# Kernel optimization log

Measured on AMD Instinct MI355X. Metric: run time of the kernel, lower is better.

The kernel has to match this reference:

```python
import jax, jax.numpy as jnp
import numpy as np

NEG_RATIO = 3.0
IOU_THR = 0.5
ALPHA = 1.0


def _cxcywh_to_xyxy(b):
    return jnp.concatenate([b[..., :2] - b[..., 2:] / 2, b[..., :2] + b[..., 2:] / 2], -1)


def _box_iou(a, b):  # a: [G,4] xyxy, b: [A,4] xyxy -> [G,A]
    lt = jnp.maximum(a[:, None, :2], b[None, :, :2])
    rb = jnp.minimum(a[:, None, 2:], b[None, :, 2:])
    wh = jnp.clip(rb - lt, 0.0)
    inter = wh[..., 0] * wh[..., 1]
    area_a = (a[:, 2] - a[:, 0]) * (a[:, 3] - a[:, 1])
    area_b = (b[:, 2] - b[:, 0]) * (b[:, 3] - b[:, 1])
    return inter / (area_a[:, None] + area_b[None, :] - inter)


def _encode(gt, anc):  # both cxcywh, last dim 4
    g_cxcy = (gt[..., :2] - anc[..., :2]) / anc[..., 2:]
    g_wh = jnp.log(gt[..., 2:]) - jnp.log(anc[..., 2:])
    return jnp.concatenate([g_cxcy, g_wh], -1)


def _match_one(boxes, labels, anchors):
    # boxes: [G,4] cxcywh, labels: [G] int, anchors: [A,4] cxcywh -> [A,5]
    ious = _box_iou(_cxcywh_to_xyxy(boxes), _cxcywh_to_xyxy(anchors))  # [G,A]
    best_gt_ov = ious.max(0)
    best_gt_idx = ious.argmax(0)  # [A]
    over = best_gt_ov > IOU_THR  # [A]
    lab_f = labels.astype(anchors.dtype)
    # anchors over threshold take their best gt, encoded w.r.t. that anchor
    enc_per_anchor = _encode(boxes[best_gt_idx], anchors)  # [A,4]
    ph = jnp.where(over[:, None],
                   jnp.concatenate([enc_per_anchor, lab_f[best_gt_idx][:, None]], -1),
                   0.0)  # [A,5]
    # every gt also claims its best anchor
    best_prior_idx = ious.argmax(1)  # [G]
    enc_best = _encode(boxes, anchors[best_prior_idx])  # [G,4]
    y2 = jnp.concatenate([enc_best, lab_f[:, None]], -1)
    return ph.at[best_prior_idx].set(y2)


def _multibox_loss(loc_pred, conf_pred, anchors, gt_boxes, gt_labels):
    B, A, C = conf_pred.shape
    target = jax.vmap(_match_one, in_axes=(0, 0, None))(gt_boxes, gt_labels, anchors)  # [B,A,5]
    pos = (target[:, :, 4:5] > 0).astype(loc_pred.dtype)  # [B,A,1]
    num_pos = pos.sum(axis=1, keepdims=True)  # [B,1,1]
    N = pos.sum()
    # smooth L1 on masked locations (beta=1), sum reduction
    d = pos * loc_pred - pos * target[:, :, :4]
    ad = jnp.abs(d)
    loc_loss = jnp.where(ad < 1.0, 0.5 * d * d, ad - 0.5).sum()
    # hard negative mining
    num_neg = jnp.minimum(NEG_RATIO * num_pos, A - 1)  # [B,1,1]
    lse = jax.scipy.special.logsumexp(conf_pred, axis=-1, keepdims=True)  # [B,A,1]
    idx01 = (target[:, :, 4:5] != 0).astype(jnp.int32)  # faithful: gathers class 0 or 1
    gathered = jnp.take_along_axis(conf_pred, idx01, axis=-1)  # [B,A,1]
    cls_l = (lse - gathered) * (1.0 - pos)  # zero-out positives
    order = jnp.argsort(-cls_l, axis=1)  # descending sort indices
    rank = jnp.argsort(order, axis=1)  # rank of each box's loss
    neg_mask = rank < num_neg
    sampled = jnp.logical_or(pos > 0, neg_mask)  # [B,A,1]
    s = sampled.astype(conf_pred.dtype)
    logits = (s * conf_pred).reshape(-1, C)
    labels_ce = (s * target[:, :, 4:5]).reshape(-1).astype(jnp.int32)
    lse2 = jax.scipy.special.logsumexp(logits, axis=-1)
    picked = jnp.take_along_axis(logits, labels_ce[:, None], axis=1)[:, 0]
    cls_loss = (lse2 - picked).sum()
    return (loc_loss + ALPHA * cls_loss) / N


def setup_inputs() -> dict:
    key = jax.random.key(0)
    k1, k2, k3, k4, k5, k6, k7 = jax.random.split(key, 7)
    B, A, C, G = 64, 8732, 81, 32
    loc_pred = jax.random.normal(k1, (B, A, 4), jnp.float32)
    conf_pred = jax.random.normal(k2, (B, A, C), jnp.float32)
    anc_cxcy = jax.random.uniform(k3, (A, 2), jnp.float32)
    anc_wh = jax.random.uniform(k4, (A, 2), jnp.float32) * 0.48 + 0.02
    anchors = jnp.concatenate([anc_cxcy, anc_wh], -1)
    gt_cxcy = jax.random.uniform(k5, (B, G, 2), jnp.float32) * 0.8 + 0.1
    gt_wh = jax.random.uniform(k6, (B, G, 2), jnp.float32) * 0.35 + 0.05
    gt_boxes = jnp.concatenate([gt_cxcy, gt_wh], -1)
    gt_labels = jax.random.randint(k7, (B, G), 0, C - 1, jnp.int32) + 1  # labels in 1..C-1
    return {"loc_pred": loc_pred, "conf_pred": conf_pred, "anchors": anchors,
            "gt_boxes": gt_boxes, "gt_labels": gt_labels}


def reference(loc_pred, conf_pred, anchors, gt_boxes, gt_labels):
    return _multibox_loss(loc_pred, conf_pred, anchors, gt_boxes, gt_labels)
```

## Files before the change

### kernel.cpp

```cpp
#include <hip/hip_runtime.h>
#include <math.h>

#pragma clang fp contract(off)

#define BB 64
#define AA 8732
#define CC 81
#define GG 32
#define A_BLOCKS 35
#define KA1_BLOCKS (BB*A_BLOCKS)
#define KA2_BLOCKS (BB*GG/4)
#define ROWS_PC 64
#define KC_BLOCKS (BB*AA/ROWS_PC)
#define CHUNK_F4 (ROWS_PC*81/4)


__global__ __launch_bounds__(256) void kAC(const float* __restrict__ anchors,
    const float* __restrict__ gt_boxes, const float* __restrict__ conf,
    unsigned char* __restrict__ bestg, unsigned int* __restrict__ bestp,
    float* __restrict__ cls_l, unsigned int* __restrict__ ticket,
    double* __restrict__ btot_acc, int* __restrict__ np_acc)
{
    __shared__ float buf[ROWS_PC * 81];
    int tid = threadIdx.x;
    if (blockIdx.x == 0 && tid == 0) {
        *ticket = 0u; *btot_acc = 0.0; *np_acc = 0;
    }
    if (blockIdx.x < KA1_BLOCKS) {
        int blk = blockIdx.x;
        int b = blk / A_BLOCKS, ca = blk % A_BLOCKS;
        int a = ca * 256 + tid;
        float4* gco = (float4*)buf;
        float* gar = buf + GG * 4;
        if (tid < GG) {
            float4 gb = ((const float4*)gt_boxes)[b * GG + tid];
            float x1 = gb.x - gb.z / 2.0f, y1 = gb.y - gb.w / 2.0f;
            float x2 = gb.x + gb.z / 2.0f, y2 = gb.y + gb.w / 2.0f;
            gco[tid] = make_float4(x1, y1, x2, y2);
            gar[tid] = (x2 - x1) * (y2 - y1);
        }
        __syncthreads();
        if (a >= AA) return;
        float4 an = ((const float4*)anchors)[a];
        float ax1 = an.x - an.z / 2.0f, ay1 = an.y - an.w / 2.0f;
        float ax2 = an.x + an.z / 2.0f, ay2 = an.y + an.w / 2.0f;
        float aar = (ax2 - ax1) * (ay2 - ay1);
        float bi = -1.0f, bu = 1.0f; int bgi = 0;
#pragma unroll
        for (int g = 0; g < GG; ++g) {
            float4 c = gco[g];
            float ltx = fmaxf(c.x, ax1), lty = fmaxf(c.y, ay1);
            float rbx = fminf(c.z, ax2), rby = fminf(c.w, ay2);
            float w = fmaxf(rbx - ltx, 0.0f), h = fmaxf(rby - lty, 0.0f);
            float inter = w * h;
            float uni = gar[g] + aar - inter;
            if (inter * bu > bi * uni) { bi = inter; bu = uni; bgi = g; }
        }
        bestg[b * AA + a] = (2.0f * bi > bu) ? (unsigned char)bgi : (unsigned char)0xFF;
    } else if (blockIdx.x < KA1_BLOCKS + KA2_BLOCKS) {
        int wv = tid >> 6, lane = tid & 63;
        int pair = (blockIdx.x - KA1_BLOCKS) * 4 + wv;
        int b = pair >> 5, g = pair & 31;
        float4 gb = ((const float4*)gt_boxes)[b * GG + g];
        float gx1 = gb.x - gb.z / 2.0f, gy1 = gb.y - gb.w / 2.0f;
        float gx2 = gb.x + gb.z / 2.0f, gy2 = gb.y + gb.w / 2.0f;
        float gar2 = (gx2 - gx1) * (gy2 - gy1);
        float bi = -1.0f, bu = 1.0f; int ba = 0;
        for (int a = lane; a < AA; a += 64) {
            float4 an = ((const float4*)anchors)[a];
            float ax1 = an.x - an.z / 2.0f, ay1 = an.y - an.w / 2.0f;
            float ax2 = an.x + an.z / 2.0f, ay2 = an.y + an.w / 2.0f;
            float aar = (ax2 - ax1) * (ay2 - ay1);
            float ltx = fmaxf(gx1, ax1), lty = fmaxf(gy1, ay1);
            float rbx = fminf(gx2, ax2), rby = fminf(gy2, ay2);
            float w = fmaxf(rbx - ltx, 0.0f), h = fmaxf(rby - lty, 0.0f);
            float inter = w * h;
            float uni = gar2 + aar - inter;
            if (inter * bu > bi * uni) { bi = inter; bu = uni; ba = a; }
        }
#pragma unroll
        for (int off = 32; off > 0; off >>= 1) {
            float oi = __shfl_down(bi, off);
            float ou = __shfl_down(bu, off);
            int   oa = __shfl_down(ba, off);
            float p1 = oi * bu, p2 = bi * ou;
            bool take = (p1 > p2) || ((p1 == p2) && (oa < ba));
            if (take) { bi = oi; bu = ou; ba = oa; }
        }
        if (lane == 0) bestp[pair] = (unsigned int)ba;
    } else {
        int chunk = blockIdx.x - KA1_BLOCKS - KA2_BLOCKS;
        const float4* __restrict__ src4 = (const float4*)conf;
        size_t base4 = (size_t)chunk * CHUNK_F4;
        float4* buf4 = (float4*)buf;
#pragma unroll
        for (int i = 0; i < 5; ++i) buf4[tid + 256 * i] = src4[base4 + tid + 256 * i];
        if (tid < CHUNK_F4 - 1280) buf4[1280 + tid] = src4[base4 + 1280 + tid];
        __syncthreads();
        int r = tid >> 2, q = tid & 3;
        const float* row = buf + r * 81;
        int kstart = (q == 0) ? 0 : 21 + (q - 1) * 20;
        float s = 0.0f;
#pragma unroll
        for (int k = 0; k < 20; ++k) s += __expf(row[kstart + k]);
        if (q == 0) s += __expf(row[20]);
        s += __shfl_xor(s, 1);
        s += __shfl_xor(s, 2);
        if (q == 0)
            cls_l[chunk * ROWS_PC + r] = __logf(s) - row[0];
    }
}

__global__ __launch_bounds__(1024) void kBDE(const float* __restrict__ anchors,
    const float* __restrict__ gt_boxes, const int* __restrict__ gt_labels,
    const float* __restrict__ loc_pred, const unsigned char* __restrict__ bestg,
    const unsigned int* __restrict__ bestp, const float* __restrict__ cls_l,
    const float* __restrict__ conf, unsigned int* __restrict__ ticket,
    double* __restrict__ btot_acc, int* __restrict__ np_acc,
    float* __restrict__ out)
{
    int b = blockIdx.x, tid = threadIdx.x;
    __shared__ int forced[AA];
    __shared__ unsigned char slab[AA];
    __shared__ unsigned int whist[16 * 256];
    __shared__ unsigned int hist[256];
    __shared__ float gcx[GG], gcy[GG], gw[GG], gh[GG];
    __shared__ int glab[GG];
    __shared__ double red_d[16];
    __shared__ int red_i[16];
    __shared__ unsigned int red_u[16];
    __shared__ unsigned int sh_prefix, sh_remaining;
    __shared__ int sh_np;
    __shared__ double sh_loc;
    unsigned int* cl = (unsigned int*)forced;

    for (int i = tid; i < AA; i += 1024) forced[i] = -1;
    if (tid < GG) {
        float4 gb = ((const float4*)gt_boxes)[b * GG + tid];
        gcx[tid] = gb.x; gcy[tid] = gb.y; gw[tid] = gb.z; gh[tid] = gb.w;
        glab[tid] = gt_labels[b * GG + tid];
    }
    __syncthreads();
    if (tid < GG)
        atomicMax(&forced[(int)bestp[b * GG + tid]], tid);
    __syncthreads();

    double lsum = 0.0; int pcount = 0;
    for (int a = tid; a < AA; a += 1024) {
        int gf = forced[a];
        int gsel;
        if (gf >= 0) gsel = gf;
        else {
            unsigned char bg = bestg[b * AA + a];
            gsel = (bg == 0xFF) ? -1 : (int)bg;
        }
        int lab = 0;
        if (gsel >= 0) {
            lab = glab[gsel];
            float4 an = ((const float4*)anchors)[a];
            float e0 = (gcx[gsel] - an.x) / an.z;
            float e1 = (gcy[gsel] - an.y) / an.w;
            float e2 = logf(gw[gsel]) - logf(an.z);
            float e3 = logf(gh[gsel]) - logf(an.w);
            float4 lp = ((const float4*)loc_pred)[b * AA + a];
            float d0 = lp.x - e0, d1 = lp.y - e1, d2 = lp.z - e2, d3 = lp.w - e3;
            float t = 0.0f, ad;
            ad = fabsf(d0); t += (ad < 1.0f) ? 0.5f * d0 * d0 : ad - 0.5f;
            ad = fabsf(d1); t += (ad < 1.0f) ? 0.5f * d1 * d1 : ad - 0.5f;
            ad = fabsf(d2); t += (ad < 1.0f) ? 0.5f * d2 * d2 : ad - 0.5f;
            ad = fabsf(d3); t += (ad < 1.0f) ? 0.5f * d3 * d3 : ad - 0.5f;
            lsum += (double)t;
            pcount++;
        }
        slab[a] = (unsigned char)lab;
    }
#pragma unroll
    for (int off = 32; off > 0; off >>= 1) {
        lsum += __shfl_down(lsum, off);
        pcount += __shfl_down(pcount, off);
    }
    if ((tid & 63) == 0) { red_d[tid >> 6] = lsum; red_i[tid >> 6] = pcount; }
    __syncthreads();
    if (tid == 0) {
        double L = 0.0; int P = 0;
        for (int w = 0; w < 16; ++w) { L += red_d[w]; P += red_i[w]; }
        sh_loc = L; sh_np = P;
    }
    __syncthreads();
    int np_ = sh_np;

    double pc = 0.0;
    const float* src = cls_l + b * AA;
    for (int i = tid; i < AA; i += 1024) {
        int lab = slab[i];
        float sv = src[i];
        if (lab > 0) {
            size_t rowb = ((size_t)(b * AA + i)) * 81;
            pc += (double)(sv + conf[rowb] - conf[rowb + lab]);
            cl[i] = 0u;
        } else {
            cl[i] = __float_as_uint(fmaxf(sv, 0.0f));
        }
    }
#pragma unroll
    for (int off = 32; off > 0; off >>= 1) pc += __shfl_down(pc, off);
    if ((tid & 63) == 0) red_d[tid >> 6] = pc;
    __syncthreads();
    double sum_pos = 0.0;
    int k = min(3 * np_, AA - 1);
    if (tid == 0) {
        for (int w = 0; w < 16; ++w) sum_pos += red_d[w];
        sh_prefix = 0u; sh_remaining = (unsigned int)k;
    }
    __syncthreads();

    double topk = 0.0;
    int p_t_pos = 0;
    if (k > 0) {
        for (int shift = 24; shift >= 0; shift -= 8) {
            for (int j = tid; j < 4096; j += 1024) whist[j] = 0u;
            __syncthreads();
            unsigned int mask = (shift == 24) ? 0u : (0xFFFFFFFFu << (shift + 8));
            unsigned int pre = sh_prefix;
            unsigned int* myh = whist + (tid >> 6) * 256;
            for (int i = tid; i < AA; i += 1024) {
                unsigned int u = cl[i];
                if ((u & mask) == pre) atomicAdd(&myh[(u >> shift) & 255], 1u);
            }
            __syncthreads();
            if (tid < 256) {
                unsigned int t = 0;
#pragma unroll
                for (int w = 0; w < 16; ++w) t += whist[w * 256 + tid];
                hist[tid] = t;
            }
            __syncthreads();
            if (tid < 64) {
                int l = tid;
                unsigned int h4 = hist[4 * l] + hist[4 * l + 1]
                                + hist[4 * l + 2] + hist[4 * l + 3];
                unsigned int S = h4;
#pragma unroll
                for (int off = 1; off < 64; off <<= 1) {
                    unsigned int o = __shfl_down(S, off);
                    S += (l + off < 64) ? o : 0u;
                }
                unsigned int rem = sh_remaining;
                unsigned long long ball = __ballot(S >= rem);
                int L = 63 - __clzll(ball);
                if (l == L) {
                    unsigned int rem2 = rem - (S - h4);
                    unsigned int c = 0;
                    for (int dd = 4 * L + 3; dd >= 4 * L; --dd) {
                        c += hist[dd];
                        if (c >= rem2) {
                            sh_prefix = pre | ((unsigned int)dd << shift);
                            sh_remaining = rem2 - (c - hist[dd]);
                            break;
                        }
                    }
                }
            }
            __syncthreads();
        }
        unsigned int vbits = sh_prefix;
        unsigned int myc = 0; double mys = 0.0;
        for (int i = tid; i < AA; i += 1024) {
            unsigned int u = cl[i];
            if (u > vbits) { myc++; mys += (double)__uint_as_float(u); }
        }
#pragma unroll
        for (int off = 32; off > 0; off >>= 1) {
            myc += __shfl_down(myc, off);
            mys += __shfl_down(mys, off);
        }
        if ((tid & 63) == 0) { red_u[tid >> 6] = myc; red_d[tid >> 6] = mys; }
        __syncthreads();
        if (tid == 0) {
            unsigned int cnt_gt = 0; double sum_gt = 0.0;
            for (int w = 0; w < 16; ++w) { cnt_gt += red_u[w]; sum_gt += red_d[w]; }
            topk = sum_gt + (double)(k - (int)cnt_gt) * (double)__uint_as_float(vbits);
            if (vbits == 0u) {
                int t = k - (int)cnt_gt, c2 = 0;
                for (int i = 0; i < AA && c2 < t; ++i) {
                    if (cl[i] == 0u) { c2++; if (slab[i] > 0) p_t_pos++; }
                }
            }
        }
    }
    if (tid == 0) {
        int unsampled = AA - np_ - k + p_t_pos;
        double clsb = sum_pos + topk + (double)unsampled * (double)logf(81.0f);
        double myb = sh_loc + clsb;
        atomicAdd(btot_acc, myb);
        atomicAdd(np_acc, np_);
        __threadfence();
        unsigned int t = atomicAdd(ticket, 1u);
        if (t == BB - 1) {
            double tt = atomicAdd(btot_acc, 0.0);
            int nn = atomicAdd(np_acc, 0);
            out[0] = (float)(tt / (double)nn);
        }
    }
}

extern "C" void kernel_launch(void* const* d_in, const int* in_sizes, int n_in,
                              void* d_out, int out_size, void* d_ws, size_t ws_size,
                              hipStream_t stream) {
    (void)in_sizes; (void)n_in; (void)out_size; (void)ws_size;
    const float* loc_pred  = (const float*)d_in[0];
    const float* conf_pred = (const float*)d_in[1];
    const float* anchors   = (const float*)d_in[2];
    const float* gt_boxes  = (const float*)d_in[3];
    const int*   gt_labels = (const int*)d_in[4];

    char* ws = (char*)d_ws;
    unsigned int*  bestp    = (unsigned int*)(ws + 0);
    unsigned char* bestg    = (unsigned char*)(ws + 8192);
    float*         cls_l    = (float*)(ws + 567040);
    unsigned int*  ticket   = (unsigned int*)(ws + 2802432);
    double*        btot_acc = (double*)(ws + 2802440);
    int*           np_acc   = (int*)(ws + 2802448);

    kAC <<<KA1_BLOCKS + KA2_BLOCKS + KC_BLOCKS, 256, 0, stream>>>(
        anchors, gt_boxes, conf_pred, bestg, bestp, cls_l, ticket, btot_acc, np_acc);
    kBDE<<<BB, 1024, 0, stream>>>(anchors, gt_boxes, gt_labels, loc_pred,
        bestg, bestp, cls_l, conf_pred, ticket, btot_acc, np_acc, (float*)d_out);
}
```

Measured before the change: 323.4 us.

## Persistent double-buffered softmax blocks, unrolled anchor scan, fused matching and wave-aggregated histogram

The log-sum-exp pass becomes a persistent grid of 768 blocks that loop over chunks, prefetching the next chunk into registers while the current one is processed from a double-buffered LDS tile. These blocks are placed first in the grid. The best-prior scan is unrolled four-wide. The second kernel drops the forced-anchor LDS array and its atomics in favour of a 32-way compare, and fuses the positive-class loss pass into the matching loop. It also replaces the 16 per-wave radix histograms with one shared histogram fed by ballot-aggregated atomics, trading more instructions per element for fewer atomic conflicts, fewer barriers and less LDS.

```diff
diff --git a/kernel.cpp b/kernel.cpp
--- a/kernel.cpp
+++ b/kernel.cpp
@@ -8,12 +8,29 @@
 #define CC 81
 #define GG 32
 #define A_BLOCKS 35
+#define KC_GRID 768
 #define KA1_BLOCKS (BB*A_BLOCKS)
 #define KA2_BLOCKS (BB*GG/4)
+#define TOT_BLOCKS (KC_GRID+KA1_BLOCKS+KA2_BLOCKS)
 #define ROWS_PC 64
-#define KC_BLOCKS (BB*AA/ROWS_PC)
+#define KC_CHUNKS (BB*AA/ROWS_PC)
 #define CHUNK_F4 (ROWS_PC*81/4)
 
+
+__device__ __forceinline__ void iou_upd(const float4 an, int a,
+    float gx1, float gy1, float gx2, float gy2, float gar2,
+    float& bi, float& bu, int& ba)
+{
+    float ax1 = an.x - an.z / 2.0f, ay1 = an.y - an.w / 2.0f;
+    float ax2 = an.x + an.z / 2.0f, ay2 = an.y + an.w / 2.0f;
+    float aar = (ax2 - ax1) * (ay2 - ay1);
+    float ltx = fmaxf(gx1, ax1), lty = fmaxf(gy1, ay1);
+    float rbx = fminf(gx2, ax2), rby = fminf(gy2, ay2);
+    float w = fmaxf(rbx - ltx, 0.0f), h = fmaxf(rby - lty, 0.0f);
+    float inter = w * h;
+    float uni = gar2 + aar - inter;
+    if (inter * bu > bi * uni) { bi = inter; bu = uni; ba = a; }
+}
 
 __global__ __launch_bounds__(256) void kAC(const float* __restrict__ anchors,
     const float* __restrict__ gt_boxes, const float* __restrict__ conf,
@@ -21,17 +38,71 @@
     float* __restrict__ cls_l, unsigned int* __restrict__ ticket,
     double* __restrict__ btot_acc, int* __restrict__ np_acc)
 {
-    __shared__ float buf[ROWS_PC * 81];
+    __shared__ float buf[2][ROWS_PC * 81];
     int tid = threadIdx.x;
     if (blockIdx.x == 0 && tid == 0) {
         *ticket = 0u; *btot_acc = 0.0; *np_acc = 0;
     }
-    if (blockIdx.x < KA1_BLOCKS) {
-        int blk = blockIdx.x;
+    if (blockIdx.x < KC_GRID) {
+        const float4* __restrict__ src4 = (const float4*)conf;
+        float4 r0, r1, r2, r3, r4, r5;
+        int c0 = blockIdx.x;
+        {
+            size_t b4 = (size_t)c0 * CHUNK_F4;
+            r0 = src4[b4 + tid];        r1 = src4[b4 + tid + 256];
+            r2 = src4[b4 + tid + 512];  r3 = src4[b4 + tid + 768];
+            r4 = src4[b4 + tid + 1024];
+            if (tid < 16) r5 = src4[b4 + tid + 1280];
+            float4* w4 = (float4*)buf[0];
+            w4[tid] = r0; w4[tid + 256] = r1; w4[tid + 512] = r2;
+            w4[tid + 768] = r3; w4[tid + 1024] = r4;
+            if (tid < 16) w4[tid + 1280] = r5;
+            if (c0 + KC_GRID < KC_CHUNKS) {
+                b4 = (size_t)(c0 + KC_GRID) * CHUNK_F4;
+                r0 = src4[b4 + tid];        r1 = src4[b4 + tid + 256];
+                r2 = src4[b4 + tid + 512];  r3 = src4[b4 + tid + 768];
+                r4 = src4[b4 + tid + 1024];
+                if (tid < 16) r5 = src4[b4 + tid + 1280];
+            }
+        }
+        int cur = 0;
+        for (int c = c0; c < KC_CHUNKS; c += KC_GRID) {
+            bool hn = (c + KC_GRID) < KC_CHUNKS;
+            __syncthreads();
+            if (hn) {
+                float4* w4 = (float4*)buf[cur ^ 1];
+                w4[tid] = r0; w4[tid + 256] = r1; w4[tid + 512] = r2;
+                w4[tid + 768] = r3; w4[tid + 1024] = r4;
+                if (tid < 16) w4[tid + 1280] = r5;
+            }
+            if (c + 2 * KC_GRID < KC_CHUNKS) {
+                size_t b4 = (size_t)(c + 2 * KC_GRID) * CHUNK_F4;
+                r0 = src4[b4 + tid];        r1 = src4[b4 + tid + 256];
+                r2 = src4[b4 + tid + 512];  r3 = src4[b4 + tid + 768];
+                r4 = src4[b4 + tid + 1024];
+                if (tid < 16) r5 = src4[b4 + tid + 1280];
+            }
+            {
+                int r = tid >> 2, q = tid & 3;
+                const float* row = buf[cur] + r * 81;
+                int kstart = (q == 0) ? 0 : 21 + (q - 1) * 20;
+                float s = 0.0f;
+#pragma unroll
+                for (int k = 0; k < 20; ++k) s += __expf(row[kstart + k]);
+                if (q == 0) s += __expf(row[20]);
+                s += __shfl_xor(s, 1);
+                s += __shfl_xor(s, 2);
+                if (q == 0)
+                    cls_l[c * ROWS_PC + r] = __logf(s) - row[0];
+            }
+            cur ^= 1;
+        }
+    } else if (blockIdx.x < KC_GRID + KA1_BLOCKS) {
+        float4* gco = (float4*)buf;
+        float* gar = ((float*)buf) + 128;
+        int blk = blockIdx.x - KC_GRID;
         int b = blk / A_BLOCKS, ca = blk % A_BLOCKS;
         int a = ca * 256 + tid;
-        float4* gco = (float4*)buf;
-        float* gar = buf + GG * 4;
         if (tid < GG) {
             float4 gb = ((const float4*)gt_boxes)[b * GG + tid];
             float x1 = gb.x - gb.z / 2.0f, y1 = gb.y - gb.w / 2.0f;
@@ -48,35 +119,39 @@
         float bi = -1.0f, bu = 1.0f; int bgi = 0;
 #pragma unroll
         for (int g = 0; g < GG; ++g) {
-            float4 c = gco[g];
-            float ltx = fmaxf(c.x, ax1), lty = fmaxf(c.y, ay1);
-            float rbx = fminf(c.z, ax2), rby = fminf(c.w, ay2);
+            float4 cbox = gco[g];
+            float ltx = fmaxf(cbox.x, ax1), lty = fmaxf(cbox.y, ay1);
+            float rbx = fminf(cbox.z, ax2), rby = fminf(cbox.w, ay2);
             float w = fmaxf(rbx - ltx, 0.0f), h = fmaxf(rby - lty, 0.0f);
             float inter = w * h;
             float uni = gar[g] + aar - inter;
             if (inter * bu > bi * uni) { bi = inter; bu = uni; bgi = g; }
         }
         bestg[b * AA + a] = (2.0f * bi > bu) ? (unsigned char)bgi : (unsigned char)0xFF;
-    } else if (blockIdx.x < KA1_BLOCKS + KA2_BLOCKS) {
+    } else {
         int wv = tid >> 6, lane = tid & 63;
-        int pair = (blockIdx.x - KA1_BLOCKS) * 4 + wv;
+        int pair = (blockIdx.x - KC_GRID - KA1_BLOCKS) * 4 + wv;
         int b = pair >> 5, g = pair & 31;
         float4 gb = ((const float4*)gt_boxes)[b * GG + g];
         float gx1 = gb.x - gb.z / 2.0f, gy1 = gb.y - gb.w / 2.0f;
         float gx2 = gb.x + gb.z / 2.0f, gy2 = gb.y + gb.w / 2.0f;
         float gar2 = (gx2 - gx1) * (gy2 - gy1);
+        const float4* __restrict__ A4 = (const float4*)anchors;
         float bi = -1.0f, bu = 1.0f; int ba = 0;
-        for (int a = lane; a < AA; a += 64) {
-            float4 an = ((const float4*)anchors)[a];
-            float ax1 = an.x - an.z / 2.0f, ay1 = an.y - an.w / 2.0f;
-            float ax2 = an.x + an.z / 2.0f, ay2 = an.y + an.w / 2.0f;
-            float aar = (ax2 - ax1) * (ay2 - ay1);
-            float ltx = fmaxf(gx1, ax1), lty = fmaxf(gy1, ay1);
-            float rbx = fminf(gx2, ax2), rby = fminf(gy2, ay2);
-            float w = fmaxf(rbx - ltx, 0.0f), h = fmaxf(rby - lty, 0.0f);
-            float inter = w * h;
-            float uni = gar2 + aar - inter;
-            if (inter * bu > bi * uni) { bi = inter; bu = uni; ba = a; }
+        for (int k0 = 0; k0 < 136; k0 += 4) {
+            int a0 = lane + 64 * k0;
+            float4 v0 = A4[a0];
+            float4 v1 = A4[a0 + 64];
+            float4 v2 = A4[a0 + 128];
+            float4 v3 = A4[a0 + 192];
+            iou_upd(v0, a0,       gx1, gy1, gx2, gy2, gar2, bi, bu, ba);
+            iou_upd(v1, a0 + 64,  gx1, gy1, gx2, gy2, gar2, bi, bu, ba);
+            iou_upd(v2, a0 + 128, gx1, gy1, gx2, gy2, gar2, bi, bu, ba);
+            iou_upd(v3, a0 + 192, gx1, gy1, gx2, gy2, gar2, bi, bu, ba);
+        }
+        if (lane < 28) {
+            int a = 8704 + lane;
+            iou_upd(A4[a], a, gx1, gy1, gx2, gy2, gar2, bi, bu, ba);
         }
 #pragma unroll
         for (int off = 32; off > 0; off >>= 1) {
@@ -88,30 +163,10 @@
             if (take) { bi = oi; bu = ou; ba = oa; }
         }
         if (lane == 0) bestp[pair] = (unsigned int)ba;
-    } else {
-        int chunk = blockIdx.x - KA1_BLOCKS - KA2_BLOCKS;
-        const float4* __restrict__ src4 = (const float4*)conf;
-        size_t base4 = (size_t)chunk * CHUNK_F4;
-        float4* buf4 = (float4*)buf;
-#pragma unroll
-        for (int i = 0; i < 5; ++i) buf4[tid + 256 * i] = src4[base4 + tid + 256 * i];
-        if (tid < CHUNK_F4 - 1280) buf4[1280 + tid] = src4[base4 + 1280 + tid];
-        __syncthreads();
-        int r = tid >> 2, q = tid & 3;
-        const float* row = buf + r * 81;
-        int kstart = (q == 0) ? 0 : 21 + (q - 1) * 20;
-        float s = 0.0f;
-#pragma unroll
-        for (int k = 0; k < 20; ++k) s += __expf(row[kstart + k]);
-        if (q == 0) s += __expf(row[20]);
-        s += __shfl_xor(s, 1);
-        s += __shfl_xor(s, 2);
-        if (q == 0)
-            cls_l[chunk * ROWS_PC + r] = __logf(s) - row[0];
     }
 }
 
-__global__ __launch_bounds__(1024) void kBDE(const float* __restrict__ anchors,
+__global__ __launch_bounds__(1024, 4) void kBE(const float* __restrict__ anchors,
     const float* __restrict__ gt_boxes, const int* __restrict__ gt_labels,
     const float* __restrict__ loc_pred, const unsigned char* __restrict__ bestg,
     const unsigned int* __restrict__ bestp, const float* __restrict__ cls_l,
@@ -119,35 +174,34 @@
     double* __restrict__ btot_acc, int* __restrict__ np_acc,
     float* __restrict__ out)
 {
-    int b = blockIdx.x, tid = threadIdx.x;
-    __shared__ int forced[AA];
+    int b = blockIdx.x, tid = threadIdx.x, lane = tid & 63;
+    __shared__ unsigned int cl[AA];
     __shared__ unsigned char slab[AA];
-    __shared__ unsigned int whist[16 * 256];
     __shared__ unsigned int hist[256];
     __shared__ float gcx[GG], gcy[GG], gw[GG], gh[GG];
     __shared__ int glab[GG];
-    __shared__ double red_d[16];
+    __shared__ unsigned int bp[GG];
+    __shared__ double red_d[16], red_p[16];
     __shared__ int red_i[16];
     __shared__ unsigned int red_u[16];
     __shared__ unsigned int sh_prefix, sh_remaining;
     __shared__ int sh_np;
-    __shared__ double sh_loc;
-    unsigned int* cl = (unsigned int*)forced;
-
-    for (int i = tid; i < AA; i += 1024) forced[i] = -1;
+    __shared__ double sh_loc, sh_pc;
+
     if (tid < GG) {
         float4 gb = ((const float4*)gt_boxes)[b * GG + tid];
         gcx[tid] = gb.x; gcy[tid] = gb.y; gw[tid] = gb.z; gh[tid] = gb.w;
         glab[tid] = gt_labels[b * GG + tid];
+        bp[tid] = bestp[b * GG + tid];
     }
     __syncthreads();
-    if (tid < GG)
-        atomicMax(&forced[(int)bestp[b * GG + tid]], tid);
-    __syncthreads();
-
-    double lsum = 0.0; int pcount = 0;
+
+    double lsum = 0.0, pc = 0.0; int pcount = 0;
     for (int a = tid; a < AA; a += 1024) {
-        int gf = forced[a];
+        int gf = -1;
+#pragma unroll
+        for (int g = 0; g < GG; ++g)
+            if (bp[g] == (unsigned int)a) gf = g;
         int gsel;
         if (gf >= 0) gsel = gf;
         else {
@@ -173,66 +227,60 @@
             pcount++;
         }
         slab[a] = (unsigned char)lab;
+        float sv = cls_l[b * AA + a];
+        if (lab > 0) {
+            size_t rowb = ((size_t)(b * AA + a)) * 81;
+            pc += (double)(sv + conf[rowb] - conf[rowb + lab]);
+            cl[a] = 0u;
+        } else {
+            cl[a] = __float_as_uint(fmaxf(sv, 0.0f));
+        }
     }
 #pragma unroll
     for (int off = 32; off > 0; off >>= 1) {
         lsum += __shfl_down(lsum, off);
+        pc += __shfl_down(pc, off);
         pcount += __shfl_down(pcount, off);
     }
-    if ((tid & 63) == 0) { red_d[tid >> 6] = lsum; red_i[tid >> 6] = pcount; }
+    if (lane == 0) { red_d[tid >> 6] = lsum; red_p[tid >> 6] = pc; red_i[tid >> 6] = pcount; }
     __syncthreads();
     if (tid == 0) {
-        double L = 0.0; int P = 0;
-        for (int w = 0; w < 16; ++w) { L += red_d[w]; P += red_i[w]; }
-        sh_loc = L; sh_np = P;
+        double L = 0.0, C = 0.0; int P = 0;
+        for (int w = 0; w < 16; ++w) { L += red_d[w]; C += red_p[w]; P += red_i[w]; }
+        sh_loc = L; sh_pc = C; sh_np = P;
+        sh_prefix = 0u;
+        sh_remaining = (unsigned int)min(3 * P, AA - 1);
     }
     __syncthreads();
     int np_ = sh_np;
-
-    double pc = 0.0;
-    const float* src = cls_l + b * AA;
-    for (int i = tid; i < AA; i += 1024) {
-        int lab = slab[i];
-        float sv = src[i];
-        if (lab > 0) {
-            size_t rowb = ((size_t)(b * AA + i)) * 81;
-            pc += (double)(sv + conf[rowb] - conf[rowb + lab]);
-            cl[i] = 0u;
-        } else {
-            cl[i] = __float_as_uint(fmaxf(sv, 0.0f));
-        }
-    }
-#pragma unroll
-    for (int off = 32; off > 0; off >>= 1) pc += __shfl_down(pc, off);
-    if ((tid & 63) == 0) red_d[tid >> 6] = pc;
-    __syncthreads();
-    double sum_pos = 0.0;
     int k = min(3 * np_, AA - 1);
-    if (tid == 0) {
-        for (int w = 0; w < 16; ++w) sum_pos += red_d[w];
-        sh_prefix = 0u; sh_remaining = (unsigned int)k;
-    }
-    __syncthreads();
 
     double topk = 0.0;
     int p_t_pos = 0;
     if (k > 0) {
         for (int shift = 24; shift >= 0; shift -= 8) {
-            for (int j = tid; j < 4096; j += 1024) whist[j] = 0u;
+            if (tid < 256) hist[tid] = 0u;
             __syncthreads();
             unsigned int mask = (shift == 24) ? 0u : (0xFFFFFFFFu << (shift + 8));
             unsigned int pre = sh_prefix;
-            unsigned int* myh = whist + (tid >> 6) * 256;
-            for (int i = tid; i < AA; i += 1024) {
-                unsigned int u = cl[i];
-                if ((u & mask) == pre) atomicAdd(&myh[(u >> shift) & 255], 1u);
-            }
-            __syncthreads();
-            if (tid < 256) {
-                unsigned int t = 0;
-#pragma unroll
-                for (int w = 0; w < 16; ++w) t += whist[w * 256 + tid];
-                hist[tid] = t;
+#pragma unroll
+            for (int it = 0; it < 9; ++it) {
+                int i = tid + it * 1024;
+                bool in = (i < AA);
+                unsigned int u = in ? cl[i] : 0u;
+                bool act = in && ((u & mask) == pre);
+                unsigned int d = (u >> shift) & 255u;
+                unsigned long long actm = __ballot(act);
+                while (actm) {
+                    int src = __builtin_ctzll(actm);
+                    unsigned int d0 = (unsigned int)__shfl((int)d, src);
+                    unsigned long long m = __ballot(act && (d == d0));
+                    int c = __popcll(m);
+                    if (c < 8) break;
+                    if (lane == src) atomicAdd(&hist[d0], (unsigned int)c);
+                    actm &= ~m;
+                }
+                if ((actm >> lane) & 1ull) atomicAdd(&hist[d], 1u);
             }
             __syncthreads();
             if (tid < 64) {
@@ -274,7 +322,7 @@
             myc += __shfl_down(myc, off);
             mys += __shfl_down(mys, off);
         }
-        if ((tid & 63) == 0) { red_u[tid >> 6] = myc; red_d[tid >> 6] = mys; }
+        if (lane == 0) { red_u[tid >> 6] = myc; red_d[tid >> 6] = mys; }
         __syncthreads();
         if (tid == 0) {
             unsigned int cnt_gt = 0; double sum_gt = 0.0;
@@ -290,7 +338,7 @@
     }
     if (tid == 0) {
         int unsampled = AA - np_ - k + p_t_pos;
-        double clsb = sum_pos + topk + (double)unsampled * (double)logf(81.0f);
+        double clsb = sh_pc + topk + (double)unsampled * (double)logf(81.0f);
         double myb = sh_loc + clsb;
         atomicAdd(btot_acc, myb);
         atomicAdd(np_acc, np_);
@@ -322,8 +370,8 @@
     double*        btot_acc = (double*)(ws + 2802440);
     int*           np_acc   = (int*)(ws + 2802448);
 
-    kAC <<<KA1_BLOCKS + KA2_BLOCKS + KC_BLOCKS, 256, 0, stream>>>(
-        anchors, gt_boxes, conf_pred, bestg, bestp, cls_l, ticket, btot_acc, np_acc);
-    kBDE<<<BB, 1024, 0, stream>>>(anchors, gt_boxes, gt_labels, loc_pred,
+    kAC<<<TOT_BLOCKS, 256, 0, stream>>>(anchors, gt_boxes, conf_pred,
+        bestg, bestp, cls_l, ticket, btot_acc, np_acc);
+    kBE<<<BB, 1024, 0, stream>>>(anchors, gt_boxes, gt_labels, loc_pred,
         bestg, bestp, cls_l, conf_pred, ticket, btot_acc, np_acc, (float*)d_out);
 }
```

Measured after the change: 316.0 us. 2.3% less time.
